# Kernel tuning notes

Measured on AMD Instinct MI355X. Metric: run time of the kernel, lower is better.

The kernel has to match this reference:

```python
import jax, jax.numpy as jnp
import numpy as np

B, S, E, H = 2, 2048, 512, 8
D = E // H  # head size = 64
LN_EPS = 1e-5


def setup_inputs() -> dict:
    key = jax.random.key(0)
    ks = jax.random.split(key, 8)
    s_in = 1.0 / np.sqrt(E)
    return {
        "x": jax.random.normal(ks[0], (B, S, E), jnp.float32),
        # per-head projection weights, stored [H, E, D] so q = x @ Wq[h]
        "Wq": jax.random.normal(ks[1], (H, E, D), jnp.float32) * s_in,
        "Wk": jax.random.normal(ks[2], (H, E, D), jnp.float32) * s_in,
        "Wv": jax.random.normal(ks[3], (H, E, D), jnp.float32) * s_in,
        "Wp": jax.random.normal(ks[4], (E, E), jnp.float32) * s_in,
        "bp": jnp.zeros((E,), jnp.float32),
        "gamma": jnp.ones((E,), jnp.float32),
        "beta": jnp.zeros((E,), jnp.float32),
        # causal mask buffer: masked_fill where mask == 0
        "mask": jnp.tril(jnp.ones((S, S), jnp.int32)),
    }


def reference(x, Wq, Wk, Wv, Wp, bp, gamma, beta, mask):
    # batched per-head projections (equivalent to the H small Linears)
    q = jnp.einsum("bse,hed->bhsd", x, Wq)
    k = jnp.einsum("bse,hed->bhsd", x, Wk)
    v = jnp.einsum("bse,hed->bhsd", x, Wv)
    # NOTE: original has NO 1/sqrt(d) scaling
    att_log = jnp.einsum("bhsd,bhtd->bhst", q, k)
    att_log = jnp.where(mask == 0, -jnp.inf, att_log)
    att = jax.nn.softmax(att_log, axis=-1)
    o = jnp.einsum("bhst,bhtd->bhsd", att, v)  # [B,H,S,D]
    # torch.cat((val, values)) prepends each head -> final order head H-1 .. 0
    o = o[:, ::-1]
    vals = o.transpose(0, 2, 1, 3).reshape(B, S, E)
    out = vals @ Wp.T + bp + x
    mu = jnp.mean(out, axis=-1, keepdims=True)
    var = jnp.var(out, axis=-1, keepdims=True)
    return (out - mu) * jax.lax.rsqrt(var + LN_EPS) * gamma + beta
```

## Files before the change

kernel.cpp:

```cpp
#include <hip/hip_runtime.h>

constexpr int Bn = 2;
constexpr int Sn = 2048;
constexpr int En = 512;
constexpr int Hn = 8;
constexpr int Dn = 64;
constexpr int Mn = Bn * Sn;

typedef short bf8 __attribute__((ext_vector_type(8)));
typedef float f32x4 __attribute__((ext_vector_type(4)));

constexpr size_t XY = (size_t)Mn * En;
constexpr size_t WT = (size_t)3 * En * En;
constexpr size_t WP = (size_t)En * En;
constexpr size_t PL = (size_t)Bn * Hn * Sn * Dn;

__device__ __forceinline__ unsigned short f2bf(float f) {
    unsigned int u = __float_as_uint(f);
    unsigned int r = 0x7FFFu + ((u >> 16) & 1u);
    return (unsigned short)((u + r) >> 16);
}
__device__ __forceinline__ float bf2f(unsigned short u) {
    return __uint_as_float(((unsigned int)u) << 16);
}
__device__ __forceinline__ void split2(float f, unsigned short& hi, unsigned short& lo) {
    hi = f2bf(f);
    lo = f2bf(f - bf2f(hi));
}

__device__ __forceinline__ void g2l16(const unsigned short* g, unsigned short* l) {
    typedef __attribute__((address_space(1))) const unsigned int gu32;
    typedef __attribute__((address_space(3))) unsigned int lu32;
    __builtin_amdgcn_global_load_lds((gu32*)(unsigned long long)g,
                                     (lu32*)(unsigned int)(unsigned long long)l,
                                     16, 0, 0);
}

__global__ __launch_bounds__(256)
void prep(const float* __restrict__ x, const float* __restrict__ Wp,
          const float* __restrict__ Wq, const float* __restrict__ Wk,
          const float* __restrict__ Wv,
          unsigned short* __restrict__ xh, unsigned short* __restrict__ xl,
          unsigned short* __restrict__ Wph, unsigned short* __restrict__ Wpl,
          unsigned short* __restrict__ Wth, unsigned short* __restrict__ Wtl)
{
    __shared__ float t[64][65];
    const int bid = blockIdx.x;
    const int tid = threadIdx.x;

    if (bid < 1152) {
        const float* src = (bid < 1024) ? x : Wp;
        unsigned short* hp = (bid < 1024) ? xh : Wph;
        unsigned short* lp = (bid < 1024) ? xl : Wpl;
        const int blk = (bid < 1024) ? bid : (bid - 1024);
        const size_t base = ((size_t)blk * 256 + tid) * 8;
        float a[8];
        *(float4*)&a[0] = *(const float4*)(src + base);
        *(float4*)&a[4] = *(const float4*)(src + base + 4);
        unsigned short h[8], l[8];
        #pragma unroll
        for (int j = 0; j < 8; ++j) split2(a[j], h[j], l[j]);
        *(bf8*)(hp + base) = *(bf8*)&h[0];
        *(bf8*)(lp + base) = *(bf8*)&l[0];
        return;
    }

    const int idx = bid - 1152;
    const int ph = idx >> 3;
    const int proj = ph >> 3, h = ph & 7;
    const int e0 = (idx & 7) * 64;
    const float* W = (proj == 0) ? Wq : (proj == 1) ? Wk : Wv;
    const float* src = W + (size_t)h * En * Dn + (size_t)e0 * Dn;

    const int er = tid >> 2, cg = (tid & 3) * 16;
    #pragma unroll
    for (int c = 0; c < 4; ++c) {
        float4 v = *(const float4*)(src + (size_t)er * Dn + cg + 4 * c);
        t[er][cg + 4 * c + 0] = v.x;
        t[er][cg + 4 * c + 1] = v.y;
        t[er][cg + 4 * c + 2] = v.z;
        t[er][cg + 4 * c + 3] = v.w;
    }
    __syncthreads();

    const int d = tid >> 2, jg = (tid & 3) * 16;
    unsigned short h16[16], l16[16];
    #pragma unroll
    for (int j = 0; j < 16; ++j) split2(t[jg + j][d], h16[j], l16[j]);
    const size_t n = (size_t)proj * 512 + h * 64 + d;
    unsigned short* dh = Wth + n * En + e0 + jg;
    unsigned short* dl = Wtl + n * En + e0 + jg;
    *(bf8*)dh       = *(bf8*)&h16[0];
    *(bf8*)(dh + 8) = *(bf8*)&h16[8];
    *(bf8*)dl       = *(bf8*)&l16[0];
    *(bf8*)(dl + 8) = *(bf8*)&l16[8];
}

__global__ __launch_bounds__(256)
void qkv_gemm(const unsigned short* __restrict__ xh,
              const unsigned short* __restrict__ xl,
              const unsigned short* __restrict__ Wth,
              const unsigned short* __restrict__ Wtl,
              unsigned short* __restrict__ qh_g,
              unsigned short* __restrict__ ql_g,
              unsigned short* __restrict__ kh_g,
              unsigned short* __restrict__ kl_g,
              unsigned short* __restrict__ vT_g)
{
    __shared__ __align__(16) unsigned char smraw[24576];
    unsigned short* ldsAh = (unsigned short*)smraw;
    unsigned short* ldsAl = ldsAh + 4096;
    unsigned short* ldsBh = ldsAl + 4096;
    unsigned short* ldsBl = ldsBh + 2048;
    float (*Cf)[68] = (float(*)[68])(smraw);

    const int tid = threadIdx.x;
    const int m0 = blockIdx.x * 128;
    const int ny = blockIdx.y;
    const int proj = ny >> 3, h = ny & 7;

    const int wave = tid >> 6, lane = tid & 63;
    const int wm = (wave >> 1) * 64, wn = (wave & 1) * 32;
    const int lm = lane & 15, quad = lane >> 4;

    const int l4r = lane >> 2;
    const int l4c = (lane & 3) * 8;
    const unsigned short* gAh0 = xh + (size_t)(m0 + wave * 32 + l4r) * En + l4c;
    const unsigned short* gAh1 = gAh0 + (size_t)16 * En;
    const unsigned short* gAl0 = xl + (size_t)(m0 + wave * 32 + l4r) * En + l4c;
    const unsigned short* gAl1 = gAl0 + (size_t)16 * En;
    const unsigned short* gBh  = Wth + (size_t)(ny * 64 + wave * 16 + l4r) * En + l4c;
    const unsigned short* gBl  = Wtl + (size_t)(ny * 64 + wave * 16 + l4r) * En + l4c;
    unsigned short* dAh0 = ldsAh + wave * 1024;
    unsigned short* dAh1 = dAh0 + 512;
    unsigned short* dAl0 = ldsAl + wave * 1024;
    unsigned short* dAl1 = dAl0 + 512;
    unsigned short* dBh  = ldsBh + wave * 512;
    unsigned short* dBl  = ldsBl + wave * 512;

    f32x4 acc[4][2];
    #pragma unroll
    for (int i = 0; i < 4; ++i)
        #pragma unroll
        for (int j = 0; j < 2; ++j) acc[i][j] = (f32x4){0.f, 0.f, 0.f, 0.f};

    for (int k0 = 0; k0 < En; k0 += 32) {
        g2l16(gAh0 + k0, dAh0);
        g2l16(gAh1 + k0, dAh1);
        g2l16(gAl0 + k0, dAl0);
        g2l16(gAl1 + k0, dAl1);
        g2l16(gBh + k0, dBh);
        g2l16(gBl + k0, dBl);
        __syncthreads();

        bf8 a_h[4], a_l[4], b_h[2], b_l[2];
        #pragma unroll
        for (int mi = 0; mi < 4; ++mi) {
            a_h[mi] = *(const bf8*)(ldsAh + (wm + mi * 16 + lm) * 32 + quad * 8);
            a_l[mi] = *(const bf8*)(ldsAl + (wm + mi * 16 + lm) * 32 + quad * 8);
        }
        #pragma unroll
        for (int ni = 0; ni < 2; ++ni) {
            b_h[ni] = *(const bf8*)(ldsBh + (wn + ni * 16 + lm) * 32 + quad * 8);
            b_l[ni] = *(const bf8*)(ldsBl + (wn + ni * 16 + lm) * 32 + quad * 8);
        }
        #pragma unroll
        for (int mi = 0; mi < 4; ++mi)
            #pragma unroll
            for (int ni = 0; ni < 2; ++ni) {
                acc[mi][ni] = __builtin_amdgcn_mfma_f32_16x16x32_bf16(a_h[mi], b_h[ni], acc[mi][ni], 0, 0, 0);
                acc[mi][ni] = __builtin_amdgcn_mfma_f32_16x16x32_bf16(a_h[mi], b_l[ni], acc[mi][ni], 0, 0, 0);
                acc[mi][ni] = __builtin_amdgcn_mfma_f32_16x16x32_bf16(a_l[mi], b_h[ni], acc[mi][ni], 0, 0, 0);
            }
        __syncthreads();
    }

    if (proj < 2) {
        unsigned short* hp = (proj == 0) ? qh_g : kh_g;
        unsigned short* lp = (proj == 0) ? ql_g : kl_g;
        #pragma unroll
        for (int p = 0; p < 2; ++p) {
            if ((wave >> 1) == p) {
                #pragma unroll
                for (int mi = 0; mi < 4; ++mi)
                    #pragma unroll
                    for (int ni = 0; ni < 2; ++ni)
                        #pragma unroll
                        for (int r = 0; r < 4; ++r)
                            Cf[mi * 16 + quad * 4 + r][wn + ni * 16 + lm] = acc[mi][ni][r];
            }
            __syncthreads();
            {
                const int lr = tid & 63;
                const int cg = (tid >> 6) * 16;
                const int m = m0 + p * 64 + lr;
                const int b = m >> 11, s = m & 2047;
                unsigned short hi[16], lo[16];
                #pragma unroll
                for (int j4 = 0; j4 < 4; ++j4) {
                    float4 v = *(const float4*)&Cf[lr][cg + 4 * j4];
                    split2(v.x, hi[4 * j4 + 0], lo[4 * j4 + 0]);
                    split2(v.y, hi[4 * j4 + 1], lo[4 * j4 + 1]);
                    split2(v.z, hi[4 * j4 + 2], lo[4 * j4 + 2]);
                    split2(v.w, hi[4 * j4 + 3], lo[4 * j4 + 3]);
                }
                const size_t base = (((size_t)(b * Hn + h) * Sn + s) * Dn) + cg;
                *(bf8*)(hp + base)     = *(bf8*)&hi[0];
                *(bf8*)(hp + base + 8) = *(bf8*)&hi[8];
                *(bf8*)(lp + base)     = *(bf8*)&lo[0];
                *(bf8*)(lp + base + 8) = *(bf8*)&lo[8];
            }
            __syncthreads();
        }
    } else {
        #pragma unroll
        for (int mi = 0; mi < 4; ++mi) {
            const int s0 = m0 + wm + mi * 16 + quad * 4;
            const int b = s0 >> 11, s = s0 & 2047;
            #pragma unroll
            for (int ni = 0; ni < 2; ++ni) {
                const int d = wn + ni * 16 + lm;
                ushort4 pk;
                pk.x = f2bf(acc[mi][ni][0]);
                pk.y = f2bf(acc[mi][ni][1]);
                pk.z = f2bf(acc[mi][ni][2]);
                pk.w = f2bf(acc[mi][ni][3]);
                *(ushort4*)(vT_g + ((size_t)(b * Hn + h) * Dn + d) * Sn + s) = pk;
            }
        }
    }
}

__global__ __launch_bounds__(256)
void attn(const unsigned short* __restrict__ qh_g,
          const unsigned short* __restrict__ ql_g,
          const unsigned short* __restrict__ kh_g,
          const unsigned short* __restrict__ kl_g,
          const unsigned short* __restrict__ vT_g,
          unsigned short* __restrict__ Op,
          float* __restrict__ ml)
{
    extern __shared__ unsigned short sm[];
    unsigned short (*khs)[72] = (unsigned short(*)[72])(sm);
    unsigned short (*kls)[72] = (unsigned short(*)[72])(sm + 4608);
    unsigned short (*vTs)[72] = (unsigned short(*)[72])(sm + 9216);
    unsigned short (*pts)[72] = (unsigned short(*)[72])(sm + 13824);
    float* alf = (float*)(sm + 18432);

    const int bidx = blockIdx.x;
    const int xcd = bidx & 7;
    const int g = bidx >> 3;
    const int bh = xcd * 2 + (g & 1);
    const int rest = g >> 1;
    const int hf = rest >> 5;
    const int a_ = rest & 31;
    const int qt = hf ? (31 - a_) : a_;
    const int n0 = (qt + 2) >> 1;
    const int its = hf ? n0 : 0;
    const int ite = hf ? (qt + 1) : n0;
    const int pslot = hf * 512 + bh * 32 + qt;

    const int tid = threadIdx.x;
    const int wave = tid >> 6, lane = tid & 63;
    const int quad = lane >> 4, lq = lane & 15;

    const unsigned short* khb = kh_g + (size_t)bh * Sn * Dn;
    const unsigned short* klb = kl_g + (size_t)bh * Sn * Dn;
    const unsigned short* vTb = vT_g + (size_t)bh * Dn * Sn;

    bf8 qfh[2], qfl[2];
    {
        const size_t qoff = ((size_t)bh * Sn + (size_t)qt * 64 + wave * 16 + lq) * Dn;
        #pragma unroll
        for (int c = 0; c < 2; ++c) {
            qfh[c] = *(const bf8*)(qh_g + qoff + c * 32 + quad * 8);
            qfl[c] = *(const bf8*)(ql_g + qoff + c * 32 + quad * 8);
        }
    }

    f32x4 accO[4];
    #pragma unroll
    for (int nj = 0; nj < 4; ++nj) accO[nj] = (f32x4){0.f, 0.f, 0.f, 0.f};
    float m = -1e30f, l = 0.f;

    const int srow = tid & 63;
    const int sdg  = tid >> 6;

    bf8 pk0, pk1, pl0, pl1, pv0, pv1;
    if (its < ite) {
        const int t0 = its * 64;
        const unsigned short* kr = khb + (size_t)(t0 + srow) * Dn + sdg * 16;
        const unsigned short* lr = klb + (size_t)(t0 + srow) * Dn + sdg * 16;
        const unsigned short* vr = vTb + (size_t)srow * Sn + t0 + sdg * 16;
        pk0 = *(const bf8*)(kr);  pk1 = *(const bf8*)(kr + 8);
        pl0 = *(const bf8*)(lr);  pl1 = *(const bf8*)(lr + 8);
        pv0 = *(const bf8*)(vr);  pv1 = *(const bf8*)(vr + 8);
    }

    for (int it = its; it < ite; ++it) {
        __syncthreads();
        *(bf8*)&khs[srow][sdg * 16]     = pk0;
        *(bf8*)&khs[srow][sdg * 16 + 8] = pk1;
        *(bf8*)&kls[srow][sdg * 16]     = pl0;
        *(bf8*)&kls[srow][sdg * 16 + 8] = pl1;
        *(bf8*)&vTs[srow][sdg * 16]     = pv0;
        *(bf8*)&vTs[srow][sdg * 16 + 8] = pv1;
        __syncthreads();

        if (it + 1 < ite) {
            const int t1 = (it + 1) * 64;
            const unsigned short* kr = khb + (size_t)(t1 + srow) * Dn + sdg * 16;
            const unsigned short* lr = klb + (size_t)(t1 + srow) * Dn + sdg * 16;
            const unsigned short* vr = vTb + (size_t)srow * Sn + t1 + sdg * 16;
            pk0 = *(const bf8*)(kr);  pk1 = *(const bf8*)(kr + 8);
            pl0 = *(const bf8*)(lr);  pl1 = *(const bf8*)(lr + 8);
            pv0 = *(const bf8*)(vr);  pv1 = *(const bf8*)(vr + 8);
        }

        f32x4 accS[4];
        #pragma unroll
        for (int mi = 0; mi < 4; ++mi) accS[mi] = (f32x4){0.f, 0.f, 0.f, 0.f};
        __builtin_amdgcn_s_setprio(1);
        #pragma unroll
        for (int mi = 0; mi < 4; ++mi) {
            #pragma unroll
            for (int c = 0; c < 2; ++c) {
                bf8 ah = *(const bf8*)&khs[mi * 16 + lq][c * 32 + quad * 8];
                bf8 al = *(const bf8*)&kls[mi * 16 + lq][c * 32 + quad * 8];
                accS[mi] = __builtin_amdgcn_mfma_f32_16x16x32_bf16(ah, qfh[c], accS[mi], 0, 0, 0);
                accS[mi] = __builtin_amdgcn_mfma_f32_16x16x32_bf16(ah, qfl[c], accS[mi], 0, 0, 0);
                accS[mi] = __builtin_amdgcn_mfma_f32_16x16x32_bf16(al, qfh[c], accS[mi], 0, 0, 0);
            }
        }
        __builtin_amdgcn_s_setprio(0);

        if (it == qt) {
            const int qrel = wave * 16 + lq;
            #pragma unroll
            for (int mi = 0; mi < 4; ++mi)
                #pragma unroll
                for (int r = 0; r < 4; ++r)
                    if (mi * 16 + quad * 4 + r > qrel) accS[mi][r] = -INFINITY;
        }

        float mt;
        {
            float t0 = fmaxf(fmaxf(accS[0][0], accS[0][1]), fmaxf(accS[0][2], accS[0][3]));
            float t1 = fmaxf(fmaxf(accS[1][0], accS[1][1]), fmaxf(accS[1][2], accS[1][3]));
            float t2 = fmaxf(fmaxf(accS[2][0], accS[2][1]), fmaxf(accS[2][2], accS[2][3]));
            float t3 = fmaxf(fmaxf(accS[3][0], accS[3][1]), fmaxf(accS[3][2], accS[3][3]));
            mt = fmaxf(fmaxf(t0, t1), fmaxf(t2, t3));
        }
        mt = fmaxf(mt, __shfl_xor(mt, 16));
        mt = fmaxf(mt, __shfl_xor(mt, 32));

        const bool defer = __all(mt <= m + 12.f);
        float mref, alpha = 1.f;
        if (defer) {
            mref = m;
        } else {
            mref = fmaxf(m, mt);
            alpha = __expf(m - mref);
        }

        float ls = 0.f;
        #pragma unroll
        for (int mi = 0; mi < 4; ++mi)
            #pragma unroll
            for (int r = 0; r < 4; ++r) {
                const float p = __expf(accS[mi][r] - mref);
                accS[mi][r] = p;
                ls += p;
            }
        ls += __shfl_xor(ls, 16);
        ls += __shfl_xor(ls, 32);
        if (defer) {
            l += ls;
        } else {
            l = l * alpha + ls;
            m = mref;
        }

        #pragma unroll
        for (int mi = 0; mi < 4; ++mi) {
            ushort4 pk;
            pk.x = f2bf(accS[mi][0]);
            pk.y = f2bf(accS[mi][1]);
            pk.z = f2bf(accS[mi][2]);
            pk.w = f2bf(accS[mi][3]);
            *(ushort4*)&pts[wave * 16 + lq][mi * 16 + quad * 4] = pk;
        }

        if (!defer) {
            if (quad == 0) alf[wave * 16 + lq] = alpha;
            float4 al4 = *(const float4*)&alf[wave * 16 + quad * 4];
            #pragma unroll
            for (int nj = 0; nj < 4; ++nj) {
                accO[nj][0] *= al4.x;
                accO[nj][1] *= al4.y;
                accO[nj][2] *= al4.z;
                accO[nj][3] *= al4.w;
            }
        }

        __builtin_amdgcn_s_setprio(1);
        #pragma unroll
        for (int c = 0; c < 2; ++c) {
            bf8 pf = *(const bf8*)&pts[wave * 16 + lq][c * 32 + quad * 8];
            #pragma unroll
            for (int nj = 0; nj < 4; ++nj) {
                bf8 vf = *(const bf8*)&vTs[nj * 16 + lq][c * 32 + quad * 8];
                accO[nj] = __builtin_amdgcn_mfma_f32_16x16x32_bf16(pf, vf, accO[nj], 0, 0, 0);
            }
        }
        __builtin_amdgcn_s_setprio(0);
    }

    if (quad == 0) {
        const size_t mi_ = ((size_t)pslot * 64 + wave * 16 + lq) * 2;
        ml[mi_]     = m;
        ml[mi_ + 1] = l;
    }
    #pragma unroll
    for (int r = 0; r < 4; ++r) {
        const int q = wave * 16 + quad * 4 + r;
        unsigned short* dst = Op + ((size_t)pslot * 64 + q) * 64;
        #pragma unroll
        for (int nj = 0; nj < 4; ++nj)
            dst[nj * 16 + lq] = f2bf(accO[nj][r]);
    }
}

__global__ __launch_bounds__(256)
void out_gemm(const unsigned short* __restrict__ Op,
              const float* __restrict__ ml,
              const unsigned short* __restrict__ Wph,
              const unsigned short* __restrict__ Wpl,
              const float* __restrict__ bp,
              const float* __restrict__ x,
              float* __restrict__ outp,
              float* __restrict__ outp2)
{
    __shared__ unsigned short Ah[64][40], Al[64][40];
    __shared__ __align__(16) unsigned short Bh[128][32], Bl[128][32];

    const int tid = threadIdx.x;
    const int m0 = blockIdx.x * 64;
    const int n0 = blockIdx.y * 128;
    const int kz = blockIdx.z;
    const int kbeg = kz * 256, kend = kbeg + 256;

    const int wave = tid >> 6, lane = tid & 63;
    const int wm = (wave >> 1) * 32, wn = (wave & 1) * 64;
    const int lm = lane & 15, quad = lane >> 4;

    const int am = tid >> 2;
    const int aks = (tid & 3) * 8;
    const int m_row = m0 + am;
    const int b_row = m_row >> 11, s_row = m_row & 2047;
    const int qt = s_row >> 6, qq = s_row & 63;

    float c0[8], c1[8];
    #pragma unroll
    for (int h = 0; h < 8; ++h) {
        const size_t base0 = (((size_t)(b_row * 8 + h) * 32 + qt) * 64 + qq) * 2;
        const size_t base1 = base0 + (size_t)512 * 64 * 2;
        const float m0_ = ml[base0], l0_ = ml[base0 + 1];
        const float m1_ = ml[base1], l1_ = ml[base1 + 1];
        const float mn = fmaxf(m0_, m1_);
        const float a0 = __expf(m0_ - mn), a1 = __expf(m1_ - mn);
        const float inv = 1.f / (a0 * l0_ + a1 * l1_);
        c0[h] = a0 * inv;
        c1[h] = a1 * inv;
    }

    const int l4r = lane >> 2;
    const int l4c = (lane & 3) * 8;
    const unsigned short* gB0h = Wph + (size_t)(n0 + wave * 32 + l4r) * En + l4c;
    const unsigned short* gB1h = gB0h + (size_t)16 * En;
    const unsigned short* gB0l = Wpl + (size_t)(n0 + wave * 32 + l4r) * En + l4c;
    const unsigned short* gB1l = gB0l + (size_t)16 * En;
    unsigned short* dB0h = &Bh[0][0] + wave * 1024;
    unsigned short* dB1h = dB0h + 512;
    unsigned short* dB0l = &Bl[0][0] + wave * 1024;
    unsigned short* dB1l = dB0l + 512;

    f32x4 acc[2][4];
    #pragma unroll
    for (int i = 0; i < 2; ++i)
        #pragma unroll
        for (int j = 0; j < 4; ++j) acc[i][j] = (f32x4){0.f, 0.f, 0.f, 0.f};

    bf8 po0, po1;
    {
        const int e0 = kbeg + aks;
        const int hh = 7 - (e0 >> 6);
        const int dd = e0 & 63;
        const size_t p0 = (((size_t)((b_row * 8 + hh) * 32 + qt)) * 64 + qq) * 64 + dd;
        po0 = *(const bf8*)(Op + p0);
        po1 = *(const bf8*)(Op + p0 + (size_t)512 * 64 * 64);
    }

    for (int k0 = kbeg; k0 < kend; k0 += 32) {
        g2l16(gB0h + k0, dB0h);
        g2l16(gB1h + k0, dB1h);
        g2l16(gB0l + k0, dB0l);
        g2l16(gB1l + k0, dB1l);
        {
            const int h_cur = 7 - ((k0 + aks) >> 6);
            const float w0 = c0[h_cur], w1 = c1[h_cur];
            unsigned short hi[8], lo[8];
            #pragma unroll
            for (int j = 0; j < 8; ++j) {
                const float v = w0 * bf2f((unsigned short)po0[j]) +
                                w1 * bf2f((unsigned short)po1[j]);
                split2(v, hi[j], lo[j]);
            }
            *(bf8*)&Ah[am][aks] = *(bf8*)&hi[0];
            *(bf8*)&Al[am][aks] = *(bf8*)&lo[0];
        }
        __syncthreads();

        if (k0 + 32 < kend) {
            const int e0 = k0 + 32 + aks;
            const int hh = 7 - (e0 >> 6);
            const int dd = e0 & 63;
            const size_t p0 = (((size_t)((b_row * 8 + hh) * 32 + qt)) * 64 + qq) * 64 + dd;
            po0 = *(const bf8*)(Op + p0);
            po1 = *(const bf8*)(Op + p0 + (size_t)512 * 64 * 64);
        }

        bf8 a_h[2], a_l[2], b_h[4], b_l[4];
        #pragma unroll
        for (int mi = 0; mi < 2; ++mi) {
            a_h[mi] = *(const bf8*)&Ah[wm + mi * 16 + lm][quad * 8];
            a_l[mi] = *(const bf8*)&Al[wm + mi * 16 + lm][quad * 8];
        }
        #pragma unroll
        for (int ni = 0; ni < 4; ++ni) {
            b_h[ni] = *(const bf8*)&Bh[wn + ni * 16 + lm][quad * 8];
            b_l[ni] = *(const bf8*)&Bl[wn + ni * 16 + lm][quad * 8];
        }
        #pragma unroll
        for (int mi = 0; mi < 2; ++mi)
            #pragma unroll
            for (int ni = 0; ni < 4; ++ni) {
                acc[mi][ni] = __builtin_amdgcn_mfma_f32_16x16x32_bf16(a_h[mi], b_h[ni], acc[mi][ni], 0, 0, 0);
                acc[mi][ni] = __builtin_amdgcn_mfma_f32_16x16x32_bf16(a_h[mi], b_l[ni], acc[mi][ni], 0, 0, 0);
                acc[mi][ni] = __builtin_amdgcn_mfma_f32_16x16x32_bf16(a_l[mi], b_h[ni], acc[mi][ni], 0, 0, 0);
            }
        __syncthreads();
    }

    float* dst = kz ? outp2 : outp;
    #pragma unroll
    for (int mi = 0; mi < 2; ++mi) {
        #pragma unroll
        for (int r = 0; r < 4; ++r) {
            const int m = m0 + wm + mi * 16 + quad * 4 + r;
            #pragma unroll
            for (int ni = 0; ni < 4; ++ni) {
                const int n = n0 + wn + ni * 16 + lm;
                const size_t idx = (size_t)m * En + n;
                const float extra = kz ? 0.f : (bp[n] + x[idx]);
                dst[idx] = acc[mi][ni][r] + extra;
            }
        }
    }
}

__global__ __launch_bounds__(256)
void ln_kernel(const float* __restrict__ outp,
               const float* __restrict__ outp2,
               const float* __restrict__ gamma,
               const float* __restrict__ beta,
               float* __restrict__ y)
{
    const int row = blockIdx.x * 4 + (threadIdx.x >> 6);
    const int lane = threadIdx.x & 63;
    const size_t off = (size_t)row * En + lane * 8;

    float a[8], b2[8];
    *(float4*)&a[0] = *(const float4*)(outp + off);
    *(float4*)&a[4] = *(const float4*)(outp + off + 4);
    *(float4*)&b2[0] = *(const float4*)(outp2 + off);
    *(float4*)&b2[4] = *(const float4*)(outp2 + off + 4);
    #pragma unroll
    for (int j = 0; j < 8; ++j) a[j] += b2[j];

    float sum = 0.f, sq = 0.f;
    #pragma unroll
    for (int j = 0; j < 8; ++j) { sum += a[j]; sq += a[j] * a[j]; }
    #pragma unroll
    for (int off_ = 1; off_ < 64; off_ <<= 1) {
        sum += __shfl_xor(sum, off_);
        sq  += __shfl_xor(sq, off_);
    }
    const float mu = sum * (1.f / 512.f);
    const float var = sq * (1.f / 512.f) - mu * mu;
    const float rs = rsqrtf(var + 1e-5f);

    const float* g = gamma + lane * 8;
    const float* be = beta + lane * 8;
    float o[8];
    #pragma unroll
    for (int j = 0; j < 8; ++j)
        o[j] = (a[j] - mu) * rs * g[j] + be[j];
    float* yr = y + off;
    *(float4*)(yr)     = *(float4*)&o[0];
    *(float4*)(yr + 4) = *(float4*)&o[4];
}

extern "C" void kernel_launch(void* const* d_in, const int* in_sizes, int n_in,
                              void* d_out, int out_size, void* d_ws, size_t ws_size,
                              hipStream_t stream)
{
    const float* x     = (const float*)d_in[0];
    const float* Wq    = (const float*)d_in[1];
    const float* Wk    = (const float*)d_in[2];
    const float* Wv    = (const float*)d_in[3];
    const float* Wp    = (const float*)d_in[4];
    const float* bp    = (const float*)d_in[5];
    const float* gamma = (const float*)d_in[6];
    const float* beta  = (const float*)d_in[7];

    float* ws   = (float*)d_ws;
    float* ml   = ws;
    float* outp = ws + XY;
    unsigned short* bfb = (unsigned short*)(ws + 2 * XY);
    unsigned short* xh  = bfb;
    unsigned short* xl  = bfb + XY;
    unsigned short* Wth = bfb + 2 * XY;
    unsigned short* Wtl = Wth + WT;
    unsigned short* Wph = Wtl + WT;
    unsigned short* Wpl = Wph + WP;
    unsigned short* qh  = Wpl + WP;
    unsigned short* ql  = qh + PL;
    unsigned short* kh  = ql + PL;
    unsigned short* kl  = kh + PL;
    unsigned short* vT  = kl + PL;
    unsigned short* Op = xh;
    float* outp2 = (float*)qh;

    const int attn_lds = 18432 * 2 + 256;
    hipFuncSetAttribute((const void*)attn,
                        hipFuncAttributeMaxDynamicSharedMemorySize, attn_lds);

    prep<<<dim3(1344), 256, 0, stream>>>(x, Wp, Wq, Wk, Wv,
                                         xh, xl, Wph, Wpl, Wth, Wtl);
    qkv_gemm<<<dim3(Mn / 128, 24), 256, 0, stream>>>(xh, xl, Wth, Wtl,
                                                     qh, ql, kh, kl, vT);
    attn<<<dim3(1024), 256, attn_lds, stream>>>(qh, ql, kh, kl, vT, Op, ml);
    out_gemm<<<dim3(Mn / 64, En / 128, 2), 256, 0, stream>>>(Op, ml, Wph, Wpl,
                                                             bp, x, outp, outp2);
    ln_kernel<<<dim3(Mn / 4), 256, 0, stream>>>(outp, outp2, gamma, beta,
                                                (float*)d_out);
}
```

Measured before the change: 175.7 us.

## Fuse output projection GEMM with LayerNorm in one full-row kernel

Replaces the split-K output GEMM and separate LayerNorm kernel with a single kernel where each 512-thread block computes 16 complete rows (all 512 columns, full K) and then performs LayerNorm from LDS. This removes the fp32 partial-output round trips through global memory and one kernel launch. The cost is a thinner M tile (16 rows) that reloads the whole Wp hi/lo tile per block, no Op prefetch, a larger LDS footprint with XOR-swizzled B layout, and only one wave doing the A-tile preparation.

```diff
diff --git a/kernel.cpp b/kernel.cpp
--- a/kernel.cpp
+++ b/kernel.cpp
@@ -431,39 +431,40 @@
     }
 }
 
-__global__ __launch_bounds__(256)
-void out_gemm(const unsigned short* __restrict__ Op,
-              const float* __restrict__ ml,
-              const unsigned short* __restrict__ Wph,
-              const unsigned short* __restrict__ Wpl,
-              const float* __restrict__ bp,
-              const float* __restrict__ x,
-              float* __restrict__ outp,
-              float* __restrict__ outp2)
+__global__ __launch_bounds__(512)
+void out_ln(const unsigned short* __restrict__ Op,
+            const float* __restrict__ ml,
+            const unsigned short* __restrict__ Wph,
+            const unsigned short* __restrict__ Wpl,
+            const float* __restrict__ bp,
+            const float* __restrict__ x,
+            const float* __restrict__ gamma,
+            const float* __restrict__ beta,
+            float* __restrict__ y)
 {
-    __shared__ unsigned short Ah[64][40], Al[64][40];
-    __shared__ __align__(16) unsigned short Bh[128][32], Bl[128][32];
+    extern __shared__ __align__(16) unsigned char smo[];
+    unsigned short* ldsBh = (unsigned short*)smo;
+    unsigned short* ldsBl = (unsigned short*)(smo + 32768);
+    unsigned short (*Ah)[40] = (unsigned short(*)[40])(smo + 65536);
+    unsigned short (*Al)[40] = (unsigned short(*)[40])(smo + 66816);
+    float (*Cf)[516] = (float(*)[516])smo;
 
     const int tid = threadIdx.x;
-    const int m0 = blockIdx.x * 64;
-    const int n0 = blockIdx.y * 128;
-    const int kz = blockIdx.z;
-    const int kbeg = kz * 256, kend = kbeg + 256;
-
+    const int m0 = blockIdx.x * 16;
     const int wave = tid >> 6, lane = tid & 63;
-    const int wm = (wave >> 1) * 32, wn = (wave & 1) * 64;
     const int lm = lane & 15, quad = lane >> 4;
-
-    const int am = tid >> 2;
+    const int wn = wave * 64;
+
+    const int am  = (tid & 63) >> 2;
     const int aks = (tid & 3) * 8;
     const int m_row = m0 + am;
     const int b_row = m_row >> 11, s_row = m_row & 2047;
-    const int qt = s_row >> 6, qq = s_row & 63;
+    const int qtA = s_row >> 6, qq = s_row & 63;
 
     float c0[8], c1[8];
     #pragma unroll
     for (int h = 0; h < 8; ++h) {
-        const size_t base0 = (((size_t)(b_row * 8 + h) * 32 + qt) * 64 + qq) * 2;
+        const size_t base0 = (((size_t)(b_row * 8 + h) * 32 + qtA) * 64 + qq) * 2;
         const size_t base1 = base0 + (size_t)512 * 64 * 2;
         const float m0_ = ml[base0], l0_ = ml[base0 + 1];
         const float m1_ = ml[base1], l1_ = ml[base1 + 1];
@@ -474,46 +475,35 @@
         c1[h] = a1 * inv;
     }
 
-    const int l4r = lane >> 2;
-    const int l4c = (lane & 3) * 8;
-    const unsigned short* gB0h = Wph + (size_t)(n0 + wave * 32 + l4r) * En + l4c;
-    const unsigned short* gB1h = gB0h + (size_t)16 * En;
-    const unsigned short* gB0l = Wpl + (size_t)(n0 + wave * 32 + l4r) * En + l4c;
-    const unsigned short* gB1l = gB0l + (size_t)16 * En;
-    unsigned short* dB0h = &Bh[0][0] + wave * 1024;
-    unsigned short* dB1h = dB0h + 512;
-    unsigned short* dB0l = &Bl[0][0] + wave * 1024;
-    unsigned short* dB1l = dB0l + 512;
-
-    f32x4 acc[2][4];
-    #pragma unroll
-    for (int i = 0; i < 2; ++i)
-        #pragma unroll
-        for (int j = 0; j < 4; ++j) acc[i][j] = (f32x4){0.f, 0.f, 0.f, 0.f};
-
-    bf8 po0, po1;
-    {
-        const int e0 = kbeg + aks;
-        const int hh = 7 - (e0 >> 6);
-        const int dd = e0 & 63;
-        const size_t p0 = (((size_t)((b_row * 8 + hh) * 32 + qt)) * 64 + qq) * 64 + dd;
-        po0 = *(const bf8*)(Op + p0);
-        po1 = *(const bf8*)(Op + p0 + (size_t)512 * 64 * 64);
-    }
-
-    for (int k0 = kbeg; k0 < kend; k0 += 32) {
-        g2l16(gB0h + k0, dB0h);
-        g2l16(gB1h + k0, dB1h);
-        g2l16(gB0l + k0, dB0l);
-        g2l16(gB1l + k0, dB1l);
-        {
-            const int h_cur = 7 - ((k0 + aks) >> 6);
-            const float w0 = c0[h_cur], w1 = c1[h_cur];
+    const int brow_in_ch = lane >> 2;
+    const int bslice     = lane & 3;
+
+    f32x4 acc[4];
+    #pragma unroll
+    for (int j = 0; j < 4; ++j) acc[j] = (f32x4){0.f, 0.f, 0.f, 0.f};
+
+    for (int k0 = 0; k0 < En; k0 += 32) {
+        #pragma unroll
+        for (int i = 0; i < 4; ++i) {
+            const int ch = wave * 4 + i;
+            const int n = ch * 16 + brow_in_ch;
+            const int sl = bslice ^ ((n >> 1) & 3);
+            g2l16(Wph + (size_t)n * En + k0 + sl * 8, ldsBh + ch * 512);
+            g2l16(Wpl + (size_t)n * En + k0 + sl * 8, ldsBl + ch * 512);
+        }
+        if (tid < 64) {
+            const int e0 = k0 + aks;
+            const int hh = 7 - (e0 >> 6);
+            const int dd = e0 & 63;
+            const size_t p0 = (((size_t)((b_row * 8 + hh) * 32 + qtA)) * 64 + qq) * 64 + dd;
+            bf8 o0 = *(const bf8*)(Op + p0);
+            bf8 o1 = *(const bf8*)(Op + p0 + (size_t)512 * 64 * 64);
+            const float w0 = c0[hh], w1 = c1[hh];
             unsigned short hi[8], lo[8];
             #pragma unroll
             for (int j = 0; j < 8; ++j) {
-                const float v = w0 * bf2f((unsigned short)po0[j]) +
-                                w1 * bf2f((unsigned short)po1[j]);
+                const float v = w0 * bf2f((unsigned short)o0[j]) +
+                                w1 * bf2f((unsigned short)o1[j]);
                 split2(v, hi[j], lo[j]);
             }
             *(bf8*)&Ah[am][aks] = *(bf8*)&hi[0];
@@ -521,94 +511,61 @@
         }
         __syncthreads();
 
-        if (k0 + 32 < kend) {
-            const int e0 = k0 + 32 + aks;
-            const int hh = 7 - (e0 >> 6);
-            const int dd = e0 & 63;
-            const size_t p0 = (((size_t)((b_row * 8 + hh) * 32 + qt)) * 64 + qq) * 64 + dd;
-            po0 = *(const bf8*)(Op + p0);
-            po1 = *(const bf8*)(Op + p0 + (size_t)512 * 64 * 64);
-        }
-
-        bf8 a_h[2], a_l[2], b_h[4], b_l[4];
-        #pragma unroll
-        for (int mi = 0; mi < 2; ++mi) {
-            a_h[mi] = *(const bf8*)&Ah[wm + mi * 16 + lm][quad * 8];
-            a_l[mi] = *(const bf8*)&Al[wm + mi * 16 + lm][quad * 8];
-        }
+        const bf8 a_h = *(const bf8*)&Ah[lm][quad * 8];
+        const bf8 a_l = *(const bf8*)&Al[lm][quad * 8];
         #pragma unroll
         for (int ni = 0; ni < 4; ++ni) {
-            b_h[ni] = *(const bf8*)&Bh[wn + ni * 16 + lm][quad * 8];
-            b_l[ni] = *(const bf8*)&Bl[wn + ni * 16 + lm][quad * 8];
-        }
-        #pragma unroll
-        for (int mi = 0; mi < 2; ++mi)
-            #pragma unroll
-            for (int ni = 0; ni < 4; ++ni) {
-                acc[mi][ni] = __builtin_amdgcn_mfma_f32_16x16x32_bf16(a_h[mi], b_h[ni], acc[mi][ni], 0, 0, 0);
-                acc[mi][ni] = __builtin_amdgcn_mfma_f32_16x16x32_bf16(a_h[mi], b_l[ni], acc[mi][ni], 0, 0, 0);
-                acc[mi][ni] = __builtin_amdgcn_mfma_f32_16x16x32_bf16(a_l[mi], b_h[ni], acc[mi][ni], 0, 0, 0);
-            }
+            const int n = wn + ni * 16 + lm;
+            const int sq = (quad ^ ((n >> 1) & 3)) * 8;
+            const bf8 b_h = *(const bf8*)(ldsBh + n * 32 + sq);
+            const bf8 b_l = *(const bf8*)(ldsBl + n * 32 + sq);
+            acc[ni] = __builtin_amdgcn_mfma_f32_16x16x32_bf16(a_h, b_h, acc[ni], 0, 0, 0);
+            acc[ni] = __builtin_amdgcn_mfma_f32_16x16x32_bf16(a_h, b_l, acc[ni], 0, 0, 0);
+            acc[ni] = __builtin_amdgcn_mfma_f32_16x16x32_bf16(a_l, b_h, acc[ni], 0, 0, 0);
+        }
         __syncthreads();
     }
 
-    float* dst = kz ? outp2 : outp;
-    #pragma unroll
-    for (int mi = 0; mi < 2; ++mi) {
+    #pragma unroll
+    for (int ni = 0; ni < 4; ++ni) {
+        const int n = wn + ni * 16 + lm;
+        const float bpn = bp[n];
         #pragma unroll
         for (int r = 0; r < 4; ++r) {
-            const int m = m0 + wm + mi * 16 + quad * 4 + r;
-            #pragma unroll
-            for (int ni = 0; ni < 4; ++ni) {
-                const int n = n0 + wn + ni * 16 + lm;
-                const size_t idx = (size_t)m * En + n;
-                const float extra = kz ? 0.f : (bp[n] + x[idx]);
-                dst[idx] = acc[mi][ni][r] + extra;
-            }
-        }
-    }
-}
-
-__global__ __launch_bounds__(256)
-void ln_kernel(const float* __restrict__ outp,
-               const float* __restrict__ outp2,
-               const float* __restrict__ gamma,
-               const float* __restrict__ beta,
-               float* __restrict__ y)
-{
-    const int row = blockIdx.x * 4 + (threadIdx.x >> 6);
-    const int lane = threadIdx.x & 63;
-    const size_t off = (size_t)row * En + lane * 8;
-
-    float a[8], b2[8];
-    *(float4*)&a[0] = *(const float4*)(outp + off);
-    *(float4*)&a[4] = *(const float4*)(outp + off + 4);
-    *(float4*)&b2[0] = *(const float4*)(outp2 + off);
-    *(float4*)&b2[4] = *(const float4*)(outp2 + off + 4);
-    #pragma unroll
-    for (int j = 0; j < 8; ++j) a[j] += b2[j];
-
+            const int mr = quad * 4 + r;
+            Cf[mr][n] = acc[ni][r] + bpn + x[(size_t)(m0 + mr) * En + n];
+        }
+    }
+    __syncthreads();
+
+    const int rt = tid >> 5;
+    const int tg = tid & 31;
+    float v[16];
+    #pragma unroll
+    for (int j4 = 0; j4 < 4; ++j4)
+        *(float4*)&v[j4 * 4] = *(const float4*)&Cf[rt][tg * 16 + j4 * 4];
     float sum = 0.f, sq = 0.f;
     #pragma unroll
-    for (int j = 0; j < 8; ++j) { sum += a[j]; sq += a[j] * a[j]; }
-    #pragma unroll
-    for (int off_ = 1; off_ < 64; off_ <<= 1) {
-        sum += __shfl_xor(sum, off_);
-        sq  += __shfl_xor(sq, off_);
+    for (int j = 0; j < 16; ++j) { sum += v[j]; sq += v[j] * v[j]; }
+    #pragma unroll
+    for (int o = 1; o < 32; o <<= 1) {
+        sum += __shfl_xor(sum, o);
+        sq  += __shfl_xor(sq, o);
     }
     const float mu = sum * (1.f / 512.f);
     const float var = sq * (1.f / 512.f) - mu * mu;
     const float rs = rsqrtf(var + 1e-5f);
 
-    const float* g = gamma + lane * 8;
-    const float* be = beta + lane * 8;
-    float o[8];
-    #pragma unroll
-    for (int j = 0; j < 8; ++j)
-        o[j] = (a[j] - mu) * rs * g[j] + be[j];
-    float* yr = y + off;
-    *(float4*)(yr)     = *(float4*)&o[0];
-    *(float4*)(yr + 4) = *(float4*)&o[4];
+    const float* g = gamma + tg * 16;
+    const float* be = beta + tg * 16;
+    float o[16];
+    #pragma unroll
+    for (int j = 0; j < 16; ++j)
+        o[j] = (v[j] - mu) * rs * g[j] + be[j];
+    float* yr = y + (size_t)(m0 + rt) * En + tg * 16;
+    #pragma unroll
+    for (int j4 = 0; j4 < 4; ++j4)
+        *(float4*)(yr + j4 * 4) = *(float4*)&o[j4 * 4];
 }
 
 extern "C" void kernel_launch(void* const* d_in, const int* in_sizes, int n_in,
@@ -626,7 +583,6 @@
 
     float* ws   = (float*)d_ws;
     float* ml   = ws;
-    float* outp = ws + XY;
     unsigned short* bfb = (unsigned short*)(ws + 2 * XY);
     unsigned short* xh  = bfb;
     unsigned short* xl  = bfb + XY;
@@ -640,19 +596,20 @@
     unsigned short* kl  = kh + PL;
     unsigned short* vT  = kl + PL;
     unsigned short* Op = xh;
-    float* outp2 = (float*)qh;
 
     const int attn_lds = 18432 * 2 + 256;
     hipFuncSetAttribute((const void*)attn,
                         hipFuncAttributeMaxDynamicSharedMemorySize, attn_lds);
+    const int out_lds = 68096;
+    hipFuncSetAttribute((const void*)out_ln,
+                        hipFuncAttributeMaxDynamicSharedMemorySize, out_lds);
 
     prep<<<dim3(1344), 256, 0, stream>>>(x, Wp, Wq, Wk, Wv,
                                          xh, xl, Wph, Wpl, Wth, Wtl);
     qkv_gemm<<<dim3(Mn / 128, 24), 256, 0, stream>>>(xh, xl, Wth, Wtl,
                                                      qh, ql, kh, kl, vT);
     attn<<<dim3(1024), 256, attn_lds, stream>>>(qh, ql, kh, kl, vT, Op, ml);
-    out_gemm<<<dim3(Mn / 64, En / 128, 2), 256, 0, stream>>>(Op, ml, Wph, Wpl,
-                                                             bp, x, outp, outp2);
-    ln_kernel<<<dim3(Mn / 4), 256, 0, stream>>>(outp, outp2, gamma, beta,
-                                                (float*)d_out);
-}
+    out_ln<<<dim3(Mn / 16), 512, out_lds, stream>>>(Op, ml, Wph, Wpl,
+                                                    bp, x, gamma, beta,
+                                                    (float*)d_out);
+}
```

Result: slower. 184.8 us (+5.2%).

## Widen attention blocks to 128 query rows sharing each staged K/V tile

Applied to the files above, without the earlier changes.

The attention kernel now runs 512-thread blocks (8 waves) covering two 64-row query tiles, so each staged K/V tile in LDS is reused by twice as many query rows and global K/V traffic per query falls. The grid is halved and the split-KV halves are re-derived per 128-row tile. Waves whose diagonal tile is already done skip compute with a continue but still join the barriers. The pts buffer grows for 8 waves, which costs more LDS per block and adds some load imbalance between the two query sub-tiles.

```diff
diff --git a/kernel.cpp b/kernel.cpp
--- a/kernel.cpp
+++ b/kernel.cpp
@@ -231,7 +231,7 @@
     }
 }
 
-__global__ __launch_bounds__(256)
+__global__ __launch_bounds__(512, 4)
 void attn(const unsigned short* __restrict__ qh_g,
           const unsigned short* __restrict__ ql_g,
           const unsigned short* __restrict__ kh_g,
@@ -245,24 +245,27 @@
     unsigned short (*kls)[72] = (unsigned short(*)[72])(sm + 4608);
     unsigned short (*vTs)[72] = (unsigned short(*)[72])(sm + 9216);
     unsigned short (*pts)[72] = (unsigned short(*)[72])(sm + 13824);
-    float* alf = (float*)(sm + 18432);
+    float* alf = (float*)(sm + 23040);
 
     const int bidx = blockIdx.x;
     const int xcd = bidx & 7;
     const int g = bidx >> 3;
     const int bh = xcd * 2 + (g & 1);
     const int rest = g >> 1;
-    const int hf = rest >> 5;
-    const int a_ = rest & 31;
-    const int qt = hf ? (31 - a_) : a_;
-    const int n0 = (qt + 2) >> 1;
-    const int its = hf ? n0 : 0;
-    const int ite = hf ? (qt + 1) : n0;
-    const int pslot = hf * 512 + bh * 32 + qt;
+    const int hf = rest >> 4;
+    const int a_ = rest & 15;
+    const int qt = hf ? (15 - a_) : a_;
+    const int its = hf ? (qt + 1) : 0;
+    const int ite = hf ? (2 * qt + 2) : (qt + 1);
 
     const int tid = threadIdx.x;
     const int wave = tid >> 6, lane = tid & 63;
     const int quad = lane >> 4, lq = lane & 15;
+    const int wq = wave >> 2;
+    const int w4 = wave & 3;
+    const int qt64 = 2 * qt + wq;
+    const int pslot = hf * 512 + bh * 32 + qt64;
+    const int dt = qt64;
 
     const unsigned short* khb = kh_g + (size_t)bh * Sn * Dn;
     const unsigned short* klb = kl_g + (size_t)bh * Sn * Dn;
@@ -270,7 +273,7 @@
 
     bf8 qfh[2], qfl[2];
     {
-        const size_t qoff = ((size_t)bh * Sn + (size_t)qt * 64 + wave * 16 + lq) * Dn;
+        const size_t qoff = ((size_t)bh * Sn + (size_t)qt * 128 + wave * 16 + lq) * Dn;
         #pragma unroll
         for (int c = 0; c < 2; ++c) {
             qfh[c] = *(const bf8*)(qh_g + qoff + c * 32 + quad * 8);
@@ -286,36 +289,29 @@
     const int srow = tid & 63;
     const int sdg  = tid >> 6;
 
-    bf8 pk0, pk1, pl0, pl1, pv0, pv1;
-    if (its < ite) {
+    bf8 pk0, pl0, pv0;
+    {
         const int t0 = its * 64;
-        const unsigned short* kr = khb + (size_t)(t0 + srow) * Dn + sdg * 16;
-        const unsigned short* lr = klb + (size_t)(t0 + srow) * Dn + sdg * 16;
-        const unsigned short* vr = vTb + (size_t)srow * Sn + t0 + sdg * 16;
-        pk0 = *(const bf8*)(kr);  pk1 = *(const bf8*)(kr + 8);
-        pl0 = *(const bf8*)(lr);  pl1 = *(const bf8*)(lr + 8);
-        pv0 = *(const bf8*)(vr);  pv1 = *(const bf8*)(vr + 8);
+        pk0 = *(const bf8*)(khb + (size_t)(t0 + srow) * Dn + sdg * 8);
+        pl0 = *(const bf8*)(klb + (size_t)(t0 + srow) * Dn + sdg * 8);
+        pv0 = *(const bf8*)(vTb + (size_t)srow * Sn + t0 + sdg * 8);
     }
 
     for (int it = its; it < ite; ++it) {
         __syncthreads();
-        *(bf8*)&khs[srow][sdg * 16]     = pk0;
-        *(bf8*)&khs[srow][sdg * 16 + 8] = pk1;
-        *(bf8*)&kls[srow][sdg * 16]     = pl0;
-        *(bf8*)&kls[srow][sdg * 16 + 8] = pl1;
-        *(bf8*)&vTs[srow][sdg * 16]     = pv0;
-        *(bf8*)&vTs[srow][sdg * 16 + 8] = pv1;
+        *(bf8*)&khs[srow][sdg * 8] = pk0;
+        *(bf8*)&kls[srow][sdg * 8] = pl0;
+        *(bf8*)&vTs[srow][sdg * 8] = pv0;
         __syncthreads();
 
         if (it + 1 < ite) {
             const int t1 = (it + 1) * 64;
-            const unsigned short* kr = khb + (size_t)(t1 + srow) * Dn + sdg * 16;
-            const unsigned short* lr = klb + (size_t)(t1 + srow) * Dn + sdg * 16;
-            const unsigned short* vr = vTb + (size_t)srow * Sn + t1 + sdg * 16;
-            pk0 = *(const bf8*)(kr);  pk1 = *(const bf8*)(kr + 8);
-            pl0 = *(const bf8*)(lr);  pl1 = *(const bf8*)(lr + 8);
-            pv0 = *(const bf8*)(vr);  pv1 = *(const bf8*)(vr + 8);
-        }
+            pk0 = *(const bf8*)(khb + (size_t)(t1 + srow) * Dn + sdg * 8);
+            pl0 = *(const bf8*)(klb + (size_t)(t1 + srow) * Dn + sdg * 8);
+            pv0 = *(const bf8*)(vTb + (size_t)srow * Sn + t1 + sdg * 8);
+        }
+
+        if (it > dt) continue;
 
         f32x4 accS[4];
         #pragma unroll
@@ -334,8 +330,8 @@
         }
         __builtin_amdgcn_s_setprio(0);
 
-        if (it == qt) {
-            const int qrel = wave * 16 + lq;
+        if (it == dt) {
+            const int qrel = w4 * 16 + lq;
             #pragma unroll
             for (int mi = 0; mi < 4; ++mi)
                 #pragma unroll
@@ -417,13 +413,13 @@
     }
 
     if (quad == 0) {
-        const size_t mi_ = ((size_t)pslot * 64 + wave * 16 + lq) * 2;
+        const size_t mi_ = ((size_t)pslot * 64 + w4 * 16 + lq) * 2;
         ml[mi_]     = m;
         ml[mi_ + 1] = l;
     }
     #pragma unroll
     for (int r = 0; r < 4; ++r) {
-        const int q = wave * 16 + quad * 4 + r;
+        const int q = w4 * 16 + quad * 4 + r;
         unsigned short* dst = Op + ((size_t)pslot * 64 + q) * 64;
         #pragma unroll
         for (int nj = 0; nj < 4; ++nj)
@@ -642,7 +638,7 @@
     unsigned short* Op = xh;
     float* outp2 = (float*)qh;
 
-    const int attn_lds = 18432 * 2 + 256;
+    const int attn_lds = 46592;
     hipFuncSetAttribute((const void*)attn,
                         hipFuncAttributeMaxDynamicSharedMemorySize, attn_lds);
 
@@ -650,7 +646,7 @@
                                          xh, xl, Wph, Wpl, Wth, Wtl);
     qkv_gemm<<<dim3(Mn / 128, 24), 256, 0, stream>>>(xh, xl, Wth, Wtl,
                                                      qh, ql, kh, kl, vT);
-    attn<<<dim3(1024), 256, attn_lds, stream>>>(qh, ql, kh, kl, vT, Op, ml);
+    attn<<<dim3(512), 512, attn_lds, stream>>>(qh, ql, kh, kl, vT, Op, ml);
     out_gemm<<<dim3(Mn / 64, En / 128, 2), 256, 0, stream>>>(Op, ml, Wph, Wpl,
                                                              bp, x, outp, outp2);
     ln_kernel<<<dim3(Mn / 4), 256, 0, stream>>>(outp, outp2, gamma, beta,
```

After: 173.9 us. Within noise of the previous version (-1.0%).
